# Performance work log

Hardware: AMD Instinct MI355X
Metric: run time of the kernel (lower is better)

Reference implementation:

```python
import jax, jax.numpy as jnp
import numpy as np
import math

D_MODEL = 1024
NUM_HEADS = 16
B, S = 4, 2048


def setup_inputs() -> dict:
    key = jax.random.key(0)
    ks = jax.random.split(key, 12)
    d = D_MODEL
    sc = 1.0 / math.sqrt(d)
    inp = {
        "q": jax.random.normal(ks[0], (B, S, d), jnp.float32),
        "k": jax.random.normal(ks[1], (B, S, d), jnp.float32),
        "v": jax.random.normal(ks[2], (B, S, d), jnp.float32),
        # causal mask, broadcast over batch and heads
        "mask": jnp.tril(jnp.ones((S, S), bool))[None, None, :, :],
        "Wq": jax.random.normal(ks[3], (d, d), jnp.float32) * sc,
        "bq": jnp.zeros((d,), jnp.float32),
        "Wk": jax.random.normal(ks[4], (d, d), jnp.float32) * sc,
        "bk": jnp.zeros((d,), jnp.float32),
        "Wv": jax.random.normal(ks[5], (d, d), jnp.float32) * sc,
        "bv": jnp.zeros((d,), jnp.float32),
        "Wo": jax.random.normal(ks[6], (d, d), jnp.float32) * sc,
        "bo": jnp.zeros((d,), jnp.float32),
    }
    return inp


def reference(q, k, v, mask, Wq, bq, Wk, bk, Wv, bv, Wo, bo):
    b, s, d = q.shape
    h = NUM_HEADS
    dk = d // h
    # QKV projections, then split heads: [B, H, S, dk]
    def split(x):
        return x.reshape(b, -1, h, dk).transpose(0, 2, 1, 3)
    Q = split(q @ Wq + bq)
    K = split(k @ Wk + bk)
    V = split(v @ Wv + bv)
    scores = jnp.einsum("bhqd,bhkd->bhqk", Q, K) / jnp.sqrt(jnp.float32(dk))
    scores = jnp.where(mask, scores, jnp.float32(-jnp.inf))
    attn = jax.nn.softmax(scores, axis=-1)  # dropout is identity in eval
    ctx = jnp.einsum("bhqk,bhkd->bhqd", attn, V)
    ctx = ctx.transpose(0, 2, 1, 3).reshape(b, -1, d)
    return ctx @ Wo + bo
```

## Files before the change

kernel.cpp:

```cpp
#include <hip/hip_runtime.h>
#include <hip/hip_bf16.h>

typedef unsigned short u16;
typedef __bf16 bf16x8 __attribute__((ext_vector_type(8)));
typedef float f32x4 __attribute__((ext_vector_type(4)));

#define D_MODEL 1024
#define NUM_HEADS 16
#define BATCH 4
#define SEQ 2048
#define DK 64
#define MROWS (BATCH * SEQ)
#define TENS (MROWS * D_MODEL)

#define GLOAD16(gp, lp) __builtin_amdgcn_global_load_lds( \
    (const __attribute__((address_space(1))) void*)(gp), \
    (__attribute__((address_space(3))) void*)(lp), 16, 0, 0)

__device__ inline u16 f2bf(float f) {
    __hip_bfloat16 h = __float2bfloat16(f);
    return *reinterpret_cast<u16*>(&h);
}

__global__ __launch_bounds__(256) void transpose4(
    const float* __restrict__ W0, const float* __restrict__ W1,
    const float* __restrict__ W2, const float* __restrict__ W3,
    u16* __restrict__ dst)
{
    __shared__ u16 tile[32][33];
    const float* in = (blockIdx.z == 0) ? W0 : (blockIdx.z == 1) ? W1
                    : (blockIdx.z == 2) ? W2 : W3;
    u16* out = dst + (size_t)blockIdx.z * (D_MODEL * D_MODEL);
    int x = blockIdx.x * 32 + threadIdx.x;
    int y = blockIdx.y * 32 + threadIdx.y;
    for (int i = 0; i < 32; i += 8)
        tile[threadIdx.y + i][threadIdx.x] = f2bf(in[(size_t)(y + i) * D_MODEL + x]);
    __syncthreads();
    x = blockIdx.y * 32 + threadIdx.x;
    y = blockIdx.x * 32 + threadIdx.y;
    for (int i = 0; i < 32; i += 8)
        out[(size_t)(y + i) * D_MODEL + x] = tile[threadIdx.x][threadIdx.y + i];
}

__global__ __launch_bounds__(256) void cvt_bf16(
    const float* __restrict__ x0, const float* __restrict__ x1,
    u16* __restrict__ dst)
{
    const float* x = blockIdx.z ? x1 : x0;
    u16* o = dst + (size_t)blockIdx.z * TENS;
    size_t i = ((size_t)blockIdx.x * 256 + threadIdx.x) * 8;
    f32x4 a = *(const f32x4*)(x + i);
    f32x4 b = *(const f32x4*)(x + i + 4);
    union { u16 s[8]; uint4 v; } u;
    for (int t = 0; t < 4; t++) { u.s[t] = f2bf(a[t]); u.s[4 + t] = f2bf(b[t]); }
    *(uint4*)(o + i) = u.v;
}

template<bool C_F32>
__global__ __launch_bounds__(256) void gemm_b(
    const u16* __restrict__ A0, const u16* __restrict__ A1,
    const u16* __restrict__ Bt0, const u16* __restrict__ Bt1,
    const float* __restrict__ bias0, const float* __restrict__ bias1,
    void* __restrict__ C0, void* __restrict__ C1)
{
    const int z = blockIdx.z;
    const u16* A    = z ? A1 : A0;
    const u16* Bt   = z ? Bt1 : Bt0;
    const float* bias = z ? bias1 : bias0;
    void* Cp        = z ? C1 : C0;
    const int K = D_MODEL, N = D_MODEL;

    __shared__ __align__(16) u16 As[128 * 32];
    __shared__ __align__(16) u16 Bs[128 * 32];

    const int tid  = threadIdx.x;
    const int lane = tid & 63;
    const int w    = tid >> 6;
    const int wr   = w >> 1, wc = w & 1;
    const int m0   = blockIdx.y * 128;
    const int n0   = blockIdx.x * 128;
    const int col_l = lane & 15;
    const int quad  = lane >> 4;
    const int koff  = quad * 8;

    const f32x4 fz = {0.f, 0.f, 0.f, 0.f};
    f32x4 acc[4][4];
    for (int i = 0; i < 4; i++)
        for (int j = 0; j < 4; j++) acc[i][j] = fz;

    for (int k0 = 0; k0 < K; k0 += 32) {
        __syncthreads();
        for (int i = 0; i < 2; i++) {
            int c   = w * 2 + i;
            int row = c * 16 + (lane >> 2);
            GLOAD16(A  + (size_t)(m0 + row) * K + k0 + (lane & 3) * 8, (char*)As + c * 1024);
            GLOAD16(Bt + (size_t)(n0 + row) * K + k0 + (lane & 3) * 8, (char*)Bs + c * 1024);
        }
        __syncthreads();

        bf16x8 af[4], bfr[4];
        for (int i = 0; i < 4; i++)
            af[i] = *(const bf16x8*)&As[(wr * 64 + i * 16 + col_l) * 32 + koff];
        for (int j = 0; j < 4; j++)
            bfr[j] = *(const bf16x8*)&Bs[(wc * 64 + j * 16 + col_l) * 32 + koff];
        for (int i = 0; i < 4; i++)
            for (int j = 0; j < 4; j++)
                acc[i][j] = __builtin_amdgcn_mfma_f32_16x16x32_bf16(
                    af[i], bfr[j], acc[i][j], 0, 0, 0);
    }

    const int row_q = quad * 4;
    for (int j = 0; j < 4; j++) {
        int colg = n0 + wc * 64 + j * 16 + col_l;
        float bv = bias[colg];
        for (int i = 0; i < 4; i++) {
            int rowg = m0 + wr * 64 + i * 16 + row_q;
            for (int r = 0; r < 4; r++) {
                float val = acc[i][j][r] + bv;
                if (C_F32)
                    ((float*)Cp)[(size_t)(rowg + r) * N + colg] = val;
                else
                    ((u16*)Cp)[(size_t)(rowg + r) * N + colg] = f2bf(val);
            }
        }
    }
}

__global__ __launch_bounds__(256) void attn_kernel(
    const u16* __restrict__ Q, const u16* __restrict__ K,
    const u16* __restrict__ V, u16* __restrict__ ctx)
{
    __shared__ __align__(16) u16 Ksf[64 * 64];
    __shared__ __align__(16) u16 Vts[64 * 64];
    __shared__ __align__(16) u16 Ps[4][16][72];

    const int tid  = threadIdx.x;
    const int lane = tid & 63;
    const int w    = tid >> 6;
    const int bh   = blockIdx.x;
    const int iy = blockIdx.y;
    const int sj = iy >> 2, jj4 = iy & 3;
    const int qt = (sj == 0) ? jj4 : (sj == 1) ? 15 - jj4
                 : (sj == 2) ? 7 - jj4 : 8 + jj4;
    const int b    = bh >> 4, h = bh & 15;
    const int q0   = qt * 128;
    const size_t rowbase = (size_t)b * SEQ;
    const int colbase = h * DK;

    const int col_l = lane & 15;
    const int quad  = lane >> 4;
    const int r0 = tid >> 3, cc0 = tid & 7, r1 = r0 + 32;

    const int c0 = w * 2, c1 = c0 + 1;
    const int krow0 = c0 * 8 + (lane >> 3), krow1 = c1 * 8 + (lane >> 3);
    const int bb0 = (lane & 7) ^ (krow0 & 7), bb1 = (lane & 7) ^ (krow1 & 7);
    const u16* Kg0 = K + (rowbase + krow0) * D_MODEL + colbase + bb0 * 8;
    const u16* Kg1 = K + (rowbase + krow1) * D_MODEL + colbase + bb1 * 8;
    u16* KsW0 = &Ksf[c0 * 512 + lane * 8];
    u16* KsW1 = &Ksf[c1 * 512 + lane * 8];
    const u16* Vg0 = V + (rowbase + r0) * D_MODEL + colbase + cc0 * 8;
    const u16* Vg1 = V + (rowbase + r1) * D_MODEL + colbase + cc0 * 8;

    bf16x8 aq[2][2];
    for (int rb = 0; rb < 2; rb++) {
        const u16* qp = Q + (rowbase + q0 + rb * 64 + w * 16 + col_l) * D_MODEL + colbase;
        aq[rb][0] = *(const bf16x8*)(qp + quad * 8);
        aq[rb][1] = *(const bf16x8*)(qp + 32 + quad * 8);
    }

    bf16x8 ones;
    for (int i = 0; i < 8; i++) ones[i] = (__bf16)1.0f;

    const f32x4 fz = {0.f, 0.f, 0.f, 0.f};
    f32x4 oacc[2][4];
    for (int rb = 0; rb < 2; rb++)
        for (int j = 0; j < 4; j++) oacc[rb][j] = fz;
    f32x4 lacc[2] = {fz, fz};

    const int ktmax = 2 * qt + 1;
    const size_t tstep = (size_t)64 * D_MODEL;

    uint4 kA0 = *(const uint4*)Kg0;
    uint4 kA1 = *(const uint4*)Kg1;
    uint4 vA0 = *(const uint4*)Vg0;
    uint4 vA1 = *(const uint4*)Vg1;

    for (int kt = 0; kt <= ktmax; kt++) {
        const int k0 = kt * 64;
        const size_t noff = (size_t)((kt < ktmax) ? kt + 1 : ktmax) * tstep;
        uint4 kB0 = *(const uint4*)(Kg0 + noff);
        uint4 kB1 = *(const uint4*)(Kg1 + noff);
        uint4 vB0 = *(const uint4*)(Vg0 + noff);
        uint4 vB1 = *(const uint4*)(Vg1 + noff);

        asm volatile("s_waitcnt lgkmcnt(0)" ::: "memory");
        __builtin_amdgcn_s_barrier();

        *(uint4*)KsW0 = kA0;
        *(uint4*)KsW1 = kA1;
        {
            union { uint4 v; u16 s[8]; } t0, t1;
            t0.v = vA0; t1.v = vA1;
            for (int jj = 0; jj < 8; jj++) {
                int fx = ((cc0 ^ jj) & 7) << 3;
                Vts[(cc0 * 8 + jj) * 64 + (r0 ^ fx)] = t0.s[jj];
                Vts[(cc0 * 8 + jj) * 64 + (r1 ^ fx)] = t1.s[jj];
            }
        }
        asm volatile("s_waitcnt lgkmcnt(0)" ::: "memory");
        __builtin_amdgcn_s_barrier();

        const bool rb0a = (kt <= 2 * qt);

        f32x4 s0acc[4], s1acc[4];
        for (int j = 0; j < 4; j++) { s0acc[j] = fz; s1acc[j] = fz; }
        __builtin_amdgcn_s_setprio(1);
        for (int j = 0; j < 4; j++) {
            int krow = j * 16 + col_l, sw = krow & 7;
            bf16x8 bk0 = *(const bf16x8*)&Ksf[krow * 64 + ((quad ^ sw) * 8)];
            bf16x8 bk1 = *(const bf16x8*)&Ksf[krow * 64 + (((4 + quad) ^ sw) * 8)];
            s0acc[j] = __builtin_amdgcn_mfma_f32_16x16x32_bf16(aq[0][0], bk0, s0acc[j], 0, 0, 0);
            s0acc[j] = __builtin_amdgcn_mfma_f32_16x16x32_bf16(aq[0][1], bk1, s0acc[j], 0, 0, 0);
            s1acc[j] = __builtin_amdgcn_mfma_f32_16x16x32_bf16(aq[1][0], bk0, s1acc[j], 0, 0, 0);
            s1acc[j] = __builtin_amdgcn_mfma_f32_16x16x32_bf16(aq[1][1], bk1, s1acc[j], 0, 0, 0);
        }
        __builtin_amdgcn_s_setprio(0);

        bf16x8 ap00, ap01, ap10, ap11;
        {
            const bool diag = (kt == 2 * qt);
            if (diag) {
                const int qg = q0 + w * 16 + quad * 4;
                for (int j = 0; j < 4; j++) {
                    int kg = k0 + j * 16 + col_l;
                    for (int r = 0; r < 4; r++) {
                        float e = __expf(s0acc[j][r] * 0.125f);
                        if (kg > qg + r) e = 0.f;
                        Ps[w][quad * 4 + r][j * 16 + col_l] = f2bf(e);
                    }
                }
            } else {
                for (int j = 0; j < 4; j++)
                    for (int r = 0; r < 4; r++)
                        Ps[w][quad * 4 + r][j * 16 + col_l] =
                            f2bf(__expf(s0acc[j][r] * 0.125f));
            }
            __threadfence_block();
            ap00 = *(const bf16x8*)&Ps[w][col_l][quad * 8];
            ap01 = *(const bf16x8*)&Ps[w][col_l][32 + quad * 8];
            if (rb0a) {
                lacc[0] = __builtin_amdgcn_mfma_f32_16x16x32_bf16(ap00, ones, lacc[0], 0, 0, 0);
                lacc[0] = __builtin_amdgcn_mfma_f32_16x16x32_bf16(ap01, ones, lacc[0], 0, 0, 0);
            }
        }
        __threadfence_block();
        {
            const bool diag = (kt == 2 * qt + 1);
            if (diag) {
                const int qg = q0 + 64 + w * 16 + quad * 4;
                for (int j = 0; j < 4; j++) {
                    int kg = k0 + j * 16 + col_l;
                    for (int r = 0; r < 4; r++) {
                        float e = __expf(s1acc[j][r] * 0.125f);
                        if (kg > qg + r) e = 0.f;
                        Ps[w][quad * 4 + r][j * 16 + col_l] = f2bf(e);
                    }
                }
            } else {
                for (int j = 0; j < 4; j++)
                    for (int r = 0; r < 4; r++)
                        Ps[w][quad * 4 + r][j * 16 + col_l] =
                            f2bf(__expf(s1acc[j][r] * 0.125f));
            }
            __threadfence_block();
            ap10 = *(const bf16x8*)&Ps[w][col_l][quad * 8];
            ap11 = *(const bf16x8*)&Ps[w][col_l][32 + quad * 8];
            lacc[1] = __builtin_amdgcn_mfma_f32_16x16x32_bf16(ap10, ones, lacc[1], 0, 0, 0);
            lacc[1] = __builtin_amdgcn_mfma_f32_16x16x32_bf16(ap11, ones, lacc[1], 0, 0, 0);
        }

        __builtin_amdgcn_s_setprio(1);
        for (int j = 0; j < 4; j++) {
            int vrow = j * 16 + col_l, sw = ((vrow >> 3) ^ vrow) & 7;
            bf16x8 bv0 = *(const bf16x8*)&Vts[vrow * 64 + ((quad ^ sw) * 8)];
            bf16x8 bv1 = *(const bf16x8*)&Vts[vrow * 64 + (((4 + quad) ^ sw) * 8)];
            if (rb0a) {
                oacc[0][j] = __builtin_amdgcn_mfma_f32_16x16x32_bf16(ap00, bv0, oacc[0][j], 0, 0, 0);
                oacc[0][j] = __builtin_amdgcn_mfma_f32_16x16x32_bf16(ap01, bv1, oacc[0][j], 0, 0, 0);
            }
            oacc[1][j] = __builtin_amdgcn_mfma_f32_16x16x32_bf16(ap10, bv0, oacc[1][j], 0, 0, 0);
            oacc[1][j] = __builtin_amdgcn_mfma_f32_16x16x32_bf16(ap11, bv1, oacc[1][j], 0, 0, 0);
        }
        __builtin_amdgcn_s_setprio(0);

        kA0 = kB0; kA1 = kB1; vA0 = vB0; vA1 = vB1;
    }

    for (int rb = 0; rb < 2; rb++) {
        for (int r = 0; r < 4; r++) {
            float inv = 1.f / lacc[rb][r];
            int rowg = q0 + rb * 64 + w * 16 + quad * 4 + r;
            for (int j = 0; j < 4; j++)
                ctx[(rowbase + rowg) * D_MODEL + colbase + j * 16 + col_l] =
                    f2bf(oacc[rb][j][r] * inv);
        }
    }
}

extern "C" void kernel_launch(void* const* d_in, const int* in_sizes, int n_in,
                              void* d_out, int out_size, void* d_ws, size_t ws_size,
                              hipStream_t stream) {
    const float* q  = (const float*)d_in[0];
    const float* k  = (const float*)d_in[1];
    const float* v  = (const float*)d_in[2];
    const float* Wq = (const float*)d_in[4];
    const float* bq = (const float*)d_in[5];
    const float* Wk = (const float*)d_in[6];
    const float* bk = (const float*)d_in[7];
    const float* Wv = (const float*)d_in[8];
    const float* bv = (const float*)d_in[9];
    const float* Wo = (const float*)d_in[10];
    const float* bo = (const float*)d_in[11];

    char* ws = (char*)d_ws;
    u16* Qb  = (u16*)(ws + (0ull  << 20));
    u16* Kb  = (u16*)(ws + (16ull << 20));
    u16* Vb  = (u16*)(ws + (32ull << 20));
    u16* WT  = (u16*)(ws + (48ull << 20));
    u16* WqT = WT + 0ull * D_MODEL * D_MODEL;
    u16* WkT = WT + 1ull * D_MODEL * D_MODEL;
    u16* WvT = WT + 2ull * D_MODEL * D_MODEL;
    u16* WoT = WT + 3ull * D_MODEL * D_MODEL;
    u16* ctx = Qb;
    u16* s0  = (u16*)d_out;
    u16* s1  = s0 + (size_t)TENS;

    transpose4<<<dim3(32, 32, 4), dim3(32, 8), 0, stream>>>(Wq, Wk, Wv, Wo, WT);

    const int cvt_blocks = TENS / (256 * 8);
    dim3 gg(D_MODEL / 128, MROWS / 128);

    cvt_bf16<<<dim3(cvt_blocks, 1, 2), 256, 0, stream>>>(q, k, s0);
    gemm_b<false><<<dim3(gg.x, gg.y, 2), 256, 0, stream>>>(
        s0, s1, WqT, WkT, bq, bk, Qb, Kb);

    cvt_bf16<<<dim3(cvt_blocks, 1, 1), 256, 0, stream>>>(v, v, s0);
    gemm_b<false><<<dim3(gg.x, gg.y, 1), 256, 0, stream>>>(
        s0, s0, WvT, WvT, bv, bv, Vb, Vb);

    attn_kernel<<<dim3(BATCH * NUM_HEADS, SEQ / 128), 256, 0, stream>>>(Qb, Kb, Vb, ctx);

    gemm_b<true><<<dim3(gg.x, gg.y, 1), 256, 0, stream>>>(
        ctx, ctx, WoT, WoT, bo, bo, d_out, d_out);
}
```

Measured before the change: 357.1 us.

## Pair mirrored 64-row query tiles per block and fold softmax scale into Q projection

Each attention block now handles two 64-row query tiles, a and 31-a, instead of a contiguous 128-row tile. Every block therefore does the same total causal work, and once the short tile's diagonal is passed, its score, softmax and PV MFMAs are skipped rather than computed and thrown away. The 1/sqrt(dk) scale moves into the Q projection epilogue, which removes a multiply per score element. Scaling Q before rounding to bf16 changes rounding slightly, and the rb0a branches add divergent code paths.

```diff
diff --git a/kernel.cpp b/kernel.cpp
--- a/kernel.cpp
+++ b/kernel.cpp
@@ -61,13 +61,15 @@
     const u16* __restrict__ A0, const u16* __restrict__ A1,
     const u16* __restrict__ Bt0, const u16* __restrict__ Bt1,
     const float* __restrict__ bias0, const float* __restrict__ bias1,
-    void* __restrict__ C0, void* __restrict__ C1)
+    void* __restrict__ C0, void* __restrict__ C1,
+    float os0, float os1)
 {
     const int z = blockIdx.z;
     const u16* A    = z ? A1 : A0;
     const u16* Bt   = z ? Bt1 : Bt0;
     const float* bias = z ? bias1 : bias0;
     void* Cp        = z ? C1 : C0;
+    const float os  = z ? os1 : os0;
     const int K = D_MODEL, N = D_MODEL;
 
     __shared__ __align__(16) u16 As[128 * 32];
@@ -116,7 +118,7 @@
         for (int i = 0; i < 4; i++) {
             int rowg = m0 + wr * 64 + i * 16 + row_q;
             for (int r = 0; r < 4; r++) {
-                float val = acc[i][j][r] + bv;
+                float val = (acc[i][j][r] + bv) * os;
                 if (C_F32)
                     ((float*)Cp)[(size_t)(rowg + r) * N + colg] = val;
                 else
@@ -138,12 +140,10 @@
     const int lane = tid & 63;
     const int w    = tid >> 6;
     const int bh   = blockIdx.x;
-    const int iy = blockIdx.y;
-    const int sj = iy >> 2, jj4 = iy & 3;
-    const int qt = (sj == 0) ? jj4 : (sj == 1) ? 15 - jj4
-                 : (sj == 2) ? 7 - jj4 : 8 + jj4;
+    const int a    = blockIdx.y;
     const int b    = bh >> 4, h = bh & 15;
-    const int q0   = qt * 128;
+    const int q0a  = a * 64;
+    const int q0b  = (31 - a) * 64;
     const size_t rowbase = (size_t)b * SEQ;
     const int colbase = h * DK;
 
@@ -162,10 +162,13 @@
     const u16* Vg1 = V + (rowbase + r1) * D_MODEL + colbase + cc0 * 8;
 
     bf16x8 aq[2][2];
-    for (int rb = 0; rb < 2; rb++) {
-        const u16* qp = Q + (rowbase + q0 + rb * 64 + w * 16 + col_l) * D_MODEL + colbase;
-        aq[rb][0] = *(const bf16x8*)(qp + quad * 8);
-        aq[rb][1] = *(const bf16x8*)(qp + 32 + quad * 8);
+    {
+        const u16* qp0 = Q + (rowbase + q0a + w * 16 + col_l) * D_MODEL + colbase;
+        aq[0][0] = *(const bf16x8*)(qp0 + quad * 8);
+        aq[0][1] = *(const bf16x8*)(qp0 + 32 + quad * 8);
+        const u16* qp1 = Q + (rowbase + q0b + w * 16 + col_l) * D_MODEL + colbase;
+        aq[1][0] = *(const bf16x8*)(qp1 + quad * 8);
+        aq[1][1] = *(const bf16x8*)(qp1 + 32 + quad * 8);
     }
 
     bf16x8 ones;
@@ -177,7 +180,7 @@
         for (int j = 0; j < 4; j++) oacc[rb][j] = fz;
     f32x4 lacc[2] = {fz, fz};
 
-    const int ktmax = 2 * qt + 1;
+    const int ktmax = 31 - a;
     const size_t tstep = (size_t)64 * D_MODEL;
 
     uint4 kA0 = *(const uint4*)Kg0;
@@ -210,31 +213,41 @@
         asm volatile("s_waitcnt lgkmcnt(0)" ::: "memory");
         __builtin_amdgcn_s_barrier();
 
-        const bool rb0a = (kt <= 2 * qt);
+        const bool rb0a = (kt <= a);
 
         f32x4 s0acc[4], s1acc[4];
         for (int j = 0; j < 4; j++) { s0acc[j] = fz; s1acc[j] = fz; }
         __builtin_amdgcn_s_setprio(1);
-        for (int j = 0; j < 4; j++) {
-            int krow = j * 16 + col_l, sw = krow & 7;
-            bf16x8 bk0 = *(const bf16x8*)&Ksf[krow * 64 + ((quad ^ sw) * 8)];
-            bf16x8 bk1 = *(const bf16x8*)&Ksf[krow * 64 + (((4 + quad) ^ sw) * 8)];
-            s0acc[j] = __builtin_amdgcn_mfma_f32_16x16x32_bf16(aq[0][0], bk0, s0acc[j], 0, 0, 0);
-            s0acc[j] = __builtin_amdgcn_mfma_f32_16x16x32_bf16(aq[0][1], bk1, s0acc[j], 0, 0, 0);
-            s1acc[j] = __builtin_amdgcn_mfma_f32_16x16x32_bf16(aq[1][0], bk0, s1acc[j], 0, 0, 0);
-            s1acc[j] = __builtin_amdgcn_mfma_f32_16x16x32_bf16(aq[1][1], bk1, s1acc[j], 0, 0, 0);
+        if (rb0a) {
+            for (int j = 0; j < 4; j++) {
+                int krow = j * 16 + col_l, sw = krow & 7;
+                bf16x8 bk0 = *(const bf16x8*)&Ksf[krow * 64 + ((quad ^ sw) * 8)];
+                bf16x8 bk1 = *(const bf16x8*)&Ksf[krow * 64 + (((4 + quad) ^ sw) * 8)];
+                s0acc[j] = __builtin_amdgcn_mfma_f32_16x16x32_bf16(aq[0][0], bk0, s0acc[j], 0, 0, 0);
+                s0acc[j] = __builtin_amdgcn_mfma_f32_16x16x32_bf16(aq[0][1], bk1, s0acc[j], 0, 0, 0);
+                s1acc[j] = __builtin_amdgcn_mfma_f32_16x16x32_bf16(aq[1][0], bk0, s1acc[j], 0, 0, 0);
+                s1acc[j] = __builtin_amdgcn_mfma_f32_16x16x32_bf16(aq[1][1], bk1, s1acc[j], 0, 0, 0);
+            }
+        } else {
+            for (int j = 0; j < 4; j++) {
+                int krow = j * 16 + col_l, sw = krow & 7;
+                bf16x8 bk0 = *(const bf16x8*)&Ksf[krow * 64 + ((quad ^ sw) * 8)];
+                bf16x8 bk1 = *(const bf16x8*)&Ksf[krow * 64 + (((4 + quad) ^ sw) * 8)];
+                s1acc[j] = __builtin_amdgcn_mfma_f32_16x16x32_bf16(aq[1][0], bk0, s1acc[j], 0, 0, 0);
+                s1acc[j] = __builtin_amdgcn_mfma_f32_16x16x32_bf16(aq[1][1], bk1, s1acc[j], 0, 0, 0);
+            }
         }
         __builtin_amdgcn_s_setprio(0);
 
-        bf16x8 ap00, ap01, ap10, ap11;
-        {
-            const bool diag = (kt == 2 * qt);
+        bf16x8 ap00 = ones, ap01 = ones;
+        if (rb0a) {
+            const bool diag = (kt == a);
             if (diag) {
-                const int qg = q0 + w * 16 + quad * 4;
+                const int qg = q0a + w * 16 + quad * 4;
                 for (int j = 0; j < 4; j++) {
                     int kg = k0 + j * 16 + col_l;
                     for (int r = 0; r < 4; r++) {
-                        float e = __expf(s0acc[j][r] * 0.125f);
+                        float e = __expf(s0acc[j][r]);
                         if (kg > qg + r) e = 0.f;
                         Ps[w][quad * 4 + r][j * 16 + col_l] = f2bf(e);
                     }
@@ -243,25 +256,24 @@
                 for (int j = 0; j < 4; j++)
                     for (int r = 0; r < 4; r++)
                         Ps[w][quad * 4 + r][j * 16 + col_l] =
-                            f2bf(__expf(s0acc[j][r] * 0.125f));
+                            f2bf(__expf(s0acc[j][r]));
             }
             __threadfence_block();
             ap00 = *(const bf16x8*)&Ps[w][col_l][quad * 8];
             ap01 = *(const bf16x8*)&Ps[w][col_l][32 + quad * 8];
-            if (rb0a) {
-                lacc[0] = __builtin_amdgcn_mfma_f32_16x16x32_bf16(ap00, ones, lacc[0], 0, 0, 0);
-                lacc[0] = __builtin_amdgcn_mfma_f32_16x16x32_bf16(ap01, ones, lacc[0], 0, 0, 0);
-            }
-        }
-        __threadfence_block();
+            lacc[0] = __builtin_amdgcn_mfma_f32_16x16x32_bf16(ap00, ones, lacc[0], 0, 0, 0);
+            lacc[0] = __builtin_amdgcn_mfma_f32_16x16x32_bf16(ap01, ones, lacc[0], 0, 0, 0);
+            __threadfence_block();
+        }
+        bf16x8 ap10, ap11;
         {
-            const bool diag = (kt == 2 * qt + 1);
+            const bool diag = (kt == ktmax);
             if (diag) {
-                const int qg = q0 + 64 + w * 16 + quad * 4;
+                const int qg = q0b + w * 16 + quad * 4;
                 for (int j = 0; j < 4; j++) {
                     int kg = k0 + j * 16 + col_l;
                     for (int r = 0; r < 4; r++) {
-                        float e = __expf(s1acc[j][r] * 0.125f);
+                        float e = __expf(s1acc[j][r]);
                         if (kg > qg + r) e = 0.f;
                         Ps[w][quad * 4 + r][j * 16 + col_l] = f2bf(e);
                     }
@@ -270,7 +282,7 @@
                 for (int j = 0; j < 4; j++)
                     for (int r = 0; r < 4; r++)
                         Ps[w][quad * 4 + r][j * 16 + col_l] =
-                            f2bf(__expf(s1acc[j][r] * 0.125f));
+                            f2bf(__expf(s1acc[j][r]));
             }
             __threadfence_block();
             ap10 = *(const bf16x8*)&Ps[w][col_l][quad * 8];
@@ -280,16 +292,24 @@
         }
 
         __builtin_amdgcn_s_setprio(1);
-        for (int j = 0; j < 4; j++) {
-            int vrow = j * 16 + col_l, sw = ((vrow >> 3) ^ vrow) & 7;
-            bf16x8 bv0 = *(const bf16x8*)&Vts[vrow * 64 + ((quad ^ sw) * 8)];
-            bf16x8 bv1 = *(const bf16x8*)&Vts[vrow * 64 + (((4 + quad) ^ sw) * 8)];
-            if (rb0a) {
+        if (rb0a) {
+            for (int j = 0; j < 4; j++) {
+                int vrow = j * 16 + col_l, sw = ((vrow >> 3) ^ vrow) & 7;
+                bf16x8 bv0 = *(const bf16x8*)&Vts[vrow * 64 + ((quad ^ sw) * 8)];
+                bf16x8 bv1 = *(const bf16x8*)&Vts[vrow * 64 + (((4 + quad) ^ sw) * 8)];
                 oacc[0][j] = __builtin_amdgcn_mfma_f32_16x16x32_bf16(ap00, bv0, oacc[0][j], 0, 0, 0);
                 oacc[0][j] = __builtin_amdgcn_mfma_f32_16x16x32_bf16(ap01, bv1, oacc[0][j], 0, 0, 0);
-            }
-            oacc[1][j] = __builtin_amdgcn_mfma_f32_16x16x32_bf16(ap10, bv0, oacc[1][j], 0, 0, 0);
-            oacc[1][j] = __builtin_amdgcn_mfma_f32_16x16x32_bf16(ap11, bv1, oacc[1][j], 0, 0, 0);
+                oacc[1][j] = __builtin_amdgcn_mfma_f32_16x16x32_bf16(ap10, bv0, oacc[1][j], 0, 0, 0);
+                oacc[1][j] = __builtin_amdgcn_mfma_f32_16x16x32_bf16(ap11, bv1, oacc[1][j], 0, 0, 0);
+            }
+        } else {
+            for (int j = 0; j < 4; j++) {
+                int vrow = j * 16 + col_l, sw = ((vrow >> 3) ^ vrow) & 7;
+                bf16x8 bv0 = *(const bf16x8*)&Vts[vrow * 64 + ((quad ^ sw) * 8)];
+                bf16x8 bv1 = *(const bf16x8*)&Vts[vrow * 64 + (((4 + quad) ^ sw) * 8)];
+                oacc[1][j] = __builtin_amdgcn_mfma_f32_16x16x32_bf16(ap10, bv0, oacc[1][j], 0, 0, 0);
+                oacc[1][j] = __builtin_amdgcn_mfma_f32_16x16x32_bf16(ap11, bv1, oacc[1][j], 0, 0, 0);
+            }
         }
         __builtin_amdgcn_s_setprio(0);
 
@@ -297,9 +317,10 @@
     }
 
     for (int rb = 0; rb < 2; rb++) {
+        const int qb = rb ? q0b : q0a;
         for (int r = 0; r < 4; r++) {
             float inv = 1.f / lacc[rb][r];
-            int rowg = q0 + rb * 64 + w * 16 + quad * 4 + r;
+            int rowg = qb + w * 16 + quad * 4 + r;
             for (int j = 0; j < 4; j++)
                 ctx[(rowbase + rowg) * D_MODEL + colbase + j * 16 + col_l] =
                     f2bf(oacc[rb][j][r] * inv);
@@ -342,14 +363,14 @@
 
     cvt_bf16<<<dim3(cvt_blocks, 1, 2), 256, 0, stream>>>(q, k, s0);
     gemm_b<false><<<dim3(gg.x, gg.y, 2), 256, 0, stream>>>(
-        s0, s1, WqT, WkT, bq, bk, Qb, Kb);
+        s0, s1, WqT, WkT, bq, bk, Qb, Kb, 0.125f, 1.0f);
 
     cvt_bf16<<<dim3(cvt_blocks, 1, 1), 256, 0, stream>>>(v, v, s0);
     gemm_b<false><<<dim3(gg.x, gg.y, 1), 256, 0, stream>>>(
-        s0, s0, WvT, WvT, bv, bv, Vb, Vb);
+        s0, s0, WvT, WvT, bv, bv, Vb, Vb, 1.0f, 1.0f);
 
     attn_kernel<<<dim3(BATCH * NUM_HEADS, SEQ / 128), 256, 0, stream>>>(Qb, Kb, Vb, ctx);
 
     gemm_b<true><<<dim3(gg.x, gg.y, 1), 256, 0, stream>>>(
-        ctx, ctx, WoT, WoT, bo, bo, d_out, d_out);
-}
+        ctx, ctx, WoT, WoT, bo, bo, d_out, d_out, 1.0f, 1.0f);
+}
```

Result: slower. 374.9 us (+5.0%).
